# Kernel tuning notes

Hardware: AMD Instinct MI355X
Metric: run time of the kernel (lower is better)

## Reference

```python
import jax, jax.numpy as jnp
import numpy as np

B, T, UNITS, OUT = 64, 512, 512, 256
N_SPEED, N_HD = 20, 50
VMIN, VMAX = 0.0, 0.5


def setup_inputs() -> dict:
    key = jax.random.key(0)
    ks = jax.random.split(key, 9)
    # vel[..., 0] = speed in [0, 0.5], vel[..., 1] = head direction in [0, 2pi]
    u = jax.random.uniform(ks[0], (B, T, 2), dtype=jnp.float32)
    vel = u * jnp.array([VMAX, 2.0 * np.pi], dtype=jnp.float32)
    r = jax.random.normal(ks[1], (B, T, 2), dtype=jnp.float32)  # target positions
    start_state = 0.01 * jax.random.normal(ks[2], (1, UNITS), dtype=jnp.float32)
    # Dense kernels: RandomNormal(0, 0.001) for inputs, identity for recurrent
    W_speed = 0.001 * jax.random.normal(ks[3], (N_SPEED, UNITS), dtype=jnp.float32)
    W_hd = 0.001 * jax.random.normal(ks[4], (N_HD, UNITS), dtype=jnp.float32)
    W_rec = jnp.eye(UNITS, dtype=jnp.float32) + 0.001 * jax.random.normal(ks[5], (UNITS, UNITS), dtype=jnp.float32)
    b_rec = jnp.zeros((UNITS,), dtype=jnp.float32)
    W_out = (1.0 / np.sqrt(UNITS)) * jax.random.normal(ks[6], (UNITS, OUT), dtype=jnp.float32)
    b_out = jnp.zeros((OUT,), dtype=jnp.float32)
    return {"vel": vel, "r": r, "start_state": start_state, "W_speed": W_speed,
            "W_hd": W_hd, "W_rec": W_rec, "b_rec": b_rec, "W_out": W_out, "b_out": b_out}


def reference(vel, r, start_state, W_speed, W_hd, W_rec, b_rec, W_out, b_out):
    f32 = jnp.float32
    speed_centers = jnp.linspace(VMIN, VMAX, N_SPEED, dtype=f32)          # (20,)
    speed_sd = (VMAX - VMIN) / N_SPEED
    hd_centers = jnp.linspace(0.0, 2.0 * np.pi, N_HD, dtype=f32)          # (50,)
    kappa = f32(2.0 * np.pi)                                              # VonMises concentration

    # RBF features for all timesteps at once (the per-step fusable chain)
    speed_feat = jnp.exp((-0.5 / speed_sd ** 2) * (vel[..., 0, None] - speed_centers) ** 2)  # (B,T,20)
    # VonMises pdf: exp(k*cos(x-mu)) / (2*pi*I0(k)); use i0e for stability
    i0e_k = jax.scipy.special.i0e(kappa)
    hd_feat = jnp.exp(kappa * (jnp.cos(vel[..., 1, None] - hd_centers) - 1.0)) / (2.0 * np.pi * i0e_k)  # (B,T,50)

    # Input drive (speed_input + hd_input + recurrent bias), precomputed for all t
    drive = speed_feat @ W_speed + hd_feat @ W_hd + b_rec  # (B,T,U)

    h0 = jnp.broadcast_to(start_state, (vel.shape[0], start_state.shape[1]))  # start_state * ones((B,1))

    def step(h, d_t):
        h_new = jax.nn.relu(h @ W_rec + d_t)
        return h_new, h_new

    _, hs = jax.lax.scan(step, h0, jnp.swapaxes(drive, 0, 1))  # (T,B,U)
    rnn_states = jnp.swapaxes(hs, 0, 1)                         # (B,T,U)

    out = jax.nn.relu(rnn_states @ W_out + b_out)               # (B,T,N)
    ta = out / jnp.sum(out + 1e-10, axis=1, keepdims=True)      # normalize over time
    pa = out / jnp.sum(out + 1e-10, axis=2, keepdims=True)      # normalize over nodes

    expected_centers = jnp.einsum('btn,btd->bnd', ta, r)        # (B,N,2)
    expected_position = jnp.einsum('btn,bnd->btd', pa, expected_centers)  # (B,T,2)
    return expected_position
```

## Files before the change

### kernel.cpp

```cpp
#include <hip/hip_runtime.h>
#include <hip/hip_bf16.h>

#define BATCH 64
#define TT 512
#define UNITS 512
#define NOUT 256
#define NSPEED 20
#define NHD 50
#define NFEAT 70

#define SPEED_COEF (-800.0f)
#define SPEED_STEP (0.5f / 19.0f)
#define HD_STEP (6.28318530718f / 49.0f)
#define KAPPA 6.2831853f
#define C_HD 0.9783857f

#define GS 4
#define CPB 128

__global__ __launch_bounds__(256) void prep_w4s_kernel(
    const float* __restrict__ W, float4* __restrict__ wp,
    unsigned* __restrict__ cnt) {
  int idx = blockIdx.x * 256 + threadIdx.x;
  int s = idx >> 14, k4 = (idx >> 7) & 127, col = idx & 127;
  int gcol = s * CPB + col;
  const float* w0 = W + (size_t)(k4 * 4) * UNITS + gcol;
  wp[idx] = make_float4(w0[0], w0[UNITS], w0[2 * UNITS], w0[3 * UNITS]);
  if (idx < BATCH)
    __hip_atomic_store(&cnt[idx * 32], 0u, __ATOMIC_RELAXED,
                       __HIP_MEMORY_SCOPE_AGENT);
}

__global__ __launch_bounds__(256) void feat_drive_kernel(
    const float* __restrict__ vel, const float* __restrict__ W_speed,
    const float* __restrict__ W_hd, const float* __restrict__ b_rec,
    float* __restrict__ drive) {
  __shared__ float feats[64][NFEAT];
  const int row0 = blockIdx.x * 64;
  const int tid = threadIdx.x;

  for (int j = tid; j < 64 * NFEAT; j += 256) {
    int row = j / NFEAT, k = j % NFEAT;
    int grow = row0 + row;
    float f;
    if (k < NSPEED) {
      float s = vel[grow * 2 + 0];
      float d = s - (float)k * SPEED_STEP;
      f = __expf(SPEED_COEF * d * d);
    } else {
      float hd = vel[grow * 2 + 1];
      float c = (float)(k - NSPEED) * HD_STEP;
      f = C_HD * __expf(KAPPA * (__cosf(hd - c) - 1.0f));
    }
    feats[row][k] = f;
  }
  __syncthreads();

  const float2* Ws2 = (const float2*)W_speed;
  const float2* Wh2 = (const float2*)W_hd;
  float2 br = ((const float2*)b_rec)[tid];

  for (int rg = 0; rg < 8; ++rg) {
    float a0[8], a1[8];
#pragma unroll
    for (int j = 0; j < 8; ++j) {
      a0[j] = br.x;
      a1[j] = br.y;
    }
#pragma unroll 4
    for (int k = 0; k < NSPEED; ++k) {
      float2 w = Ws2[k * 256 + tid];
#pragma unroll
      for (int j = 0; j < 8; ++j) {
        float f = feats[rg * 8 + j][k];
        a0[j] = fmaf(f, w.x, a0[j]);
        a1[j] = fmaf(f, w.y, a1[j]);
      }
    }
#pragma unroll 5
    for (int k = 0; k < NHD; ++k) {
      float2 w = Wh2[k * 256 + tid];
#pragma unroll
      for (int j = 0; j < 8; ++j) {
        float f = feats[rg * 8 + j][NSPEED + k];
        a0[j] = fmaf(f, w.x, a0[j]);
        a1[j] = fmaf(f, w.y, a1[j]);
      }
    }
#pragma unroll
    for (int j = 0; j < 8; ++j)
      ((float2*)drive)[(size_t)(row0 + rg * 8 + j) * 256 + tid] =
          make_float2(a0[j], a1[j]);
  }
}

__global__ __launch_bounds__(1024) void rnn_scan6_kernel(
    const float4* __restrict__ wp, const float* __restrict__ drive,
    const float* __restrict__ start_state, float* __restrict__ hstates,
    unsigned* __restrict__ cnt) {
  __shared__ __align__(16) float hf[UNITS];
  __shared__ float pt[1024];
  const int bid = blockIdx.x;
  const int b = bid & 63, s = bid >> 6;
  const int tid = threadIdx.x;
  const int col = tid & (CPB - 1);
  const int kg = tid >> 7;
  const int scol = s * CPB + col;

  float4 w[16];
  {
    const float4* base = wp + (s << 14) + (kg << 11) + col;
#pragma unroll
    for (int i = 0; i < 16; ++i) w[i] = base[i << 7];
  }
  if (tid < 128) ((float4*)hf)[tid] = ((const float4*)start_state)[tid];
  __syncthreads();

  const float* D = drive + (size_t)b * TT * UNITS;
  float* H = hstates + (size_t)b * TT * UNITS;
  unsigned* c = cnt + (b << 5);

  for (int t = 0; t < TT; ++t) {
    const float4* hv = (const float4*)hf + (kg << 4);
    float a0 = 0.f, a1 = 0.f, a2 = 0.f, a3 = 0.f;
#pragma unroll
    for (int i = 0; i < 16; ++i) {
      float4 h4 = hv[i];
      a0 = fmaf(h4.x, w[i].x, a0);
      a1 = fmaf(h4.y, w[i].y, a1);
      a2 = fmaf(h4.z, w[i].z, a2);
      a3 = fmaf(h4.w, w[i].w, a3);
    }
    pt[tid] = (a0 + a1) + (a2 + a3);
    __syncthreads();
    if (tid < 128) {
      float sum = 0.f;
#pragma unroll
      for (int j = 0; j < 8; ++j) sum += pt[col + (j << 7)];
      float hn = fmaxf(sum + D[t * UNITS + scol], 0.0f);
      __hip_atomic_store(&H[t * UNITS + scol], hn, __ATOMIC_RELAXED,
                         __HIP_MEMORY_SCOPE_AGENT);
    }
    if (t == TT - 1) break;
    __syncthreads();
    if (tid == 0) {
      __hip_atomic_fetch_add(c, 1u, __ATOMIC_RELAXED,
                             __HIP_MEMORY_SCOPE_AGENT);
      unsigned tgt = (unsigned)(GS * (t + 1));
      while (__hip_atomic_load(c, __ATOMIC_RELAXED,
                               __HIP_MEMORY_SCOPE_AGENT) < tgt)
        __builtin_amdgcn_s_sleep(1);
    }
    __syncthreads();
    asm volatile("" ::: "memory");
    if (tid < 128) {
      unsigned long long p0 = __hip_atomic_load(
          (const unsigned long long*)&H[t * UNITS + tid * 4], __ATOMIC_RELAXED,
          __HIP_MEMORY_SCOPE_AGENT);
      unsigned long long p1 = __hip_atomic_load(
          (const unsigned long long*)&H[t * UNITS + tid * 4 + 2],
          __ATOMIC_RELAXED, __HIP_MEMORY_SCOPE_AGENT);
      float2 f0 = __builtin_bit_cast(float2, p0);
      float2 f1 = __builtin_bit_cast(float2, p1);
      ((float4*)hf)[tid] = make_float4(f0.x, f0.y, f1.x, f1.y);
    }
    __syncthreads();
  }
}

__global__ __launch_bounds__(256) void out_gemm_kernel(
    const float* __restrict__ A,
    const float* __restrict__ Bm,
    const float* __restrict__ b_out,
    float* __restrict__ C) {
  __shared__ float As[16][132];
  __shared__ float Bs[16][132];
  const int bm = blockIdx.x, bn = blockIdx.y;
  const int tid = threadIdx.x;
  const int tm = tid >> 4, tn = tid & 15;

  float acc[8][8] = {{0.f}};

  for (int k0 = 0; k0 < UNITS; k0 += 16) {
    {
      int ar = tid >> 2;
      int ak = (tid & 3) << 2;
      float4 v0 = *(const float4*)&A[(size_t)(bm * 128 + ar) * 512 + k0 + ak];
      float4 v1 =
          *(const float4*)&A[(size_t)(bm * 128 + ar + 64) * 512 + k0 + ak];
      As[ak + 0][ar] = v0.x;
      As[ak + 1][ar] = v0.y;
      As[ak + 2][ar] = v0.z;
      As[ak + 3][ar] = v0.w;
      As[ak + 0][ar + 64] = v1.x;
      As[ak + 1][ar + 64] = v1.y;
      As[ak + 2][ar + 64] = v1.z;
      As[ak + 3][ar + 64] = v1.w;
      int bk = tid >> 4;
      int bc = (tid & 15) << 3;
      float4 w0 = *(const float4*)&Bm[(size_t)(k0 + bk) * 256 + bn * 128 + bc];
      float4 w1 =
          *(const float4*)&Bm[(size_t)(k0 + bk) * 256 + bn * 128 + bc + 4];
      *(float4*)&Bs[bk][bc] = w0;
      *(float4*)&Bs[bk][bc + 4] = w1;
    }
    __syncthreads();
#pragma unroll
    for (int kk = 0; kk < 16; ++kk) {
      float4 a0 = *(const float4*)&As[kk][tm * 8];
      float4 a1 = *(const float4*)&As[kk][tm * 8 + 4];
      float4 b0 = *(const float4*)&Bs[kk][tn * 8];
      float4 b1 = *(const float4*)&Bs[kk][tn * 8 + 4];
      float av[8] = {a0.x, a0.y, a0.z, a0.w, a1.x, a1.y, a1.z, a1.w};
      float bv[8] = {b0.x, b0.y, b0.z, b0.w, b1.x, b1.y, b1.z, b1.w};
#pragma unroll
      for (int i = 0; i < 8; ++i)
#pragma unroll
        for (int j = 0; j < 8; ++j) acc[i][j] = fmaf(av[i], bv[j], acc[i][j]);
    }
    __syncthreads();
  }

  float4 bo0 = *(const float4*)&b_out[bn * 128 + tn * 8];
  float4 bo1 = *(const float4*)&b_out[bn * 128 + tn * 8 + 4];
  float bo[8] = {bo0.x, bo0.y, bo0.z, bo0.w, bo1.x, bo1.y, bo1.z, bo1.w};
#pragma unroll
  for (int i = 0; i < 8; ++i) {
    int row = bm * 128 + tm * 8 + i;
    float o[8];
#pragma unroll
    for (int j = 0; j < 8; ++j) o[j] = fmaxf(acc[i][j] + bo[j], 0.0f);
    float* cp = &C[(size_t)row * 256 + bn * 128 + tn * 8];
    *(float4*)cp = make_float4(o[0], o[1], o[2], o[3]);
    *(float4*)(cp + 4) = make_float4(o[4], o[5], o[6], o[7]);
  }
}

__global__ __launch_bounds__(256) void ec_kernel(
    const float* __restrict__ out, const float* __restrict__ r,
    float* __restrict__ EC) {
  const int b = blockIdx.x, n = threadIdx.x;
  const float* ob = out + (size_t)b * TT * NOUT;
  const float2* rb = (const float2*)r + (size_t)b * TT;
  float s = 0.0f, e0 = 0.0f, e1 = 0.0f;
  for (int t = 0; t < TT; ++t) {
    float o = ob[t * NOUT + n];
    float2 rv = rb[t];
    s += o;
    e0 = fmaf(o, rv.x, e0);
    e1 = fmaf(o, rv.y, e1);
  }
  float inv = 1.0f / (s + 5.12e-8f);
  ((float2*)EC)[b * NOUT + n] = make_float2(e0 * inv, e1 * inv);
}

__global__ __launch_bounds__(256) void ep_kernel(
    const float* __restrict__ out, const float* __restrict__ EC,
    float* __restrict__ EP) {
  const int b = blockIdx.x;
  const int tid = threadIdx.x;
  const int lane = tid & 63, wave = tid >> 6;
  __shared__ float ec0[NOUT], ec1[NOUT];

  float2 e = ((const float2*)EC)[b * NOUT + tid];
  ec0[tid] = e.x;
  ec1[tid] = e.y;
  __syncthreads();

  float4 c0 = *(const float4*)&ec0[lane * 4];
  float4 c1 = *(const float4*)&ec1[lane * 4];

  const float* ob = out + (size_t)b * TT * NOUT;
  float2* epb = (float2*)EP + (size_t)b * TT;

  for (int t = wave; t < TT; t += 4) {
    float4 o = *(const float4*)&ob[t * NOUT + lane * 4];
    float s = o.x + o.y + o.z + o.w;
    float a0 = o.x * c0.x + o.y * c0.y + o.z * c0.z + o.w * c0.w;
    float a1 = o.x * c1.x + o.y * c1.y + o.z * c1.z + o.w * c1.w;
#pragma unroll
    for (int off = 32; off > 0; off >>= 1) {
      s += __shfl_down(s, off);
      a0 += __shfl_down(a0, off);
      a1 += __shfl_down(a1, off);
    }
    if (lane == 0) {
      float inv = 1.0f / (s + 2.56e-8f);
      epb[t] = make_float2(a0 * inv, a1 * inv);
    }
  }
}

extern "C" void kernel_launch(void* const* d_in, const int* in_sizes, int n_in,
                              void* d_out, int out_size, void* d_ws,
                              size_t ws_size, hipStream_t stream) {
  const float* vel = (const float*)d_in[0];
  const float* r = (const float*)d_in[1];
  const float* start_state = (const float*)d_in[2];
  const float* W_speed = (const float*)d_in[3];
  const float* W_hd = (const float*)d_in[4];
  const float* W_rec = (const float*)d_in[5];
  const float* b_rec = (const float*)d_in[6];
  const float* W_out = (const float*)d_in[7];
  const float* b_out = (const float*)d_in[8];
  float* EP = (float*)d_out;

  char* ws = (char*)d_ws;
  float* drive = (float*)ws;
  float* hstates = (float*)(ws + (size_t)67108864);
  float* outbuf = (float*)ws;
  float4* wpack = (float4*)(ws + (size_t)134217728);
  unsigned* cnt = (unsigned*)(ws + (size_t)135266304);
  float* EC = (float*)(ws + (size_t)135274496);

  prep_w4s_kernel<<<256, 256, 0, stream>>>(W_rec, wpack, cnt);
  feat_drive_kernel<<<512, 256, 0, stream>>>(vel, W_speed, W_hd, b_rec, drive);
  rnn_scan6_kernel<<<256, 1024, 0, stream>>>(wpack, drive, start_state,
                                             hstates, cnt);
  out_gemm_kernel<<<dim3(256, 2), 256, 0, stream>>>(hstates, W_out, b_out,
                                                    outbuf);
  ec_kernel<<<64, 256, 0, stream>>>(outbuf, r, EC);
  ep_kernel<<<64, 256, 0, stream>>>(outbuf, EC, EP);
}
```

Measured before the change: 1.278 ms.

## Replace counter barrier in RNN scan with poison-flag dataflow sync on hidden states

Drops the per-batch atomic counter barrier, one of the two per-step __syncthreads, and the thread-0 spin loop. A new kernel first fills the hidden-state buffer with a poison bit pattern, and each block then polls directly for the three remote 128-column slices of h_t until they are no longer poison. Its own slice is written straight into shared memory. This cuts one round trip of inter-block signalling per timestep, at the cost of an extra 64MB fill pass and of depending on the assumption that no real value equals the poison pattern.

```diff
diff --git a/kernel.cpp b/kernel.cpp
--- a/kernel.cpp
+++ b/kernel.cpp
@@ -17,18 +17,24 @@
 
 #define GS 4
 #define CPB 128
+#define POISON 0xAAAAAAAAu
+
+__global__ __launch_bounds__(256) void clear_h_kernel(uint4* __restrict__ H) {
+  size_t i = (size_t)(blockIdx.x * 256 + threadIdx.x) * 4;
+  uint4 p = make_uint4(POISON, POISON, POISON, POISON);
+  H[i + 0] = p;
+  H[i + 1] = p;
+  H[i + 2] = p;
+  H[i + 3] = p;
+}
 
 __global__ __launch_bounds__(256) void prep_w4s_kernel(
-    const float* __restrict__ W, float4* __restrict__ wp,
-    unsigned* __restrict__ cnt) {
+    const float* __restrict__ W, float4* __restrict__ wp) {
   int idx = blockIdx.x * 256 + threadIdx.x;
   int s = idx >> 14, k4 = (idx >> 7) & 127, col = idx & 127;
   int gcol = s * CPB + col;
   const float* w0 = W + (size_t)(k4 * 4) * UNITS + gcol;
   wp[idx] = make_float4(w0[0], w0[UNITS], w0[2 * UNITS], w0[3 * UNITS]);
-  if (idx < BATCH)
-    __hip_atomic_store(&cnt[idx * 32], 0u, __ATOMIC_RELAXED,
-                       __HIP_MEMORY_SCOPE_AGENT);
 }
 
 __global__ __launch_bounds__(256) void feat_drive_kernel(
@@ -94,10 +100,9 @@
   }
 }
 
-__global__ __launch_bounds__(1024) void rnn_scan6_kernel(
+__global__ __launch_bounds__(1024) void rnn_scan8_kernel(
     const float4* __restrict__ wp, const float* __restrict__ drive,
-    const float* __restrict__ start_state, float* __restrict__ hstates,
-    unsigned* __restrict__ cnt) {
+    const float* __restrict__ start_state, float* __restrict__ hstates) {
   __shared__ __align__(16) float hf[UNITS];
   __shared__ float pt[1024];
   const int bid = blockIdx.x;
@@ -105,7 +110,7 @@
   const int tid = threadIdx.x;
   const int col = tid & (CPB - 1);
   const int kg = tid >> 7;
-  const int scol = s * CPB + col;
+  const int scol = (s << 7) + col;
 
   float4 w[16];
   {
@@ -118,7 +123,6 @@
 
   const float* D = drive + (size_t)b * TT * UNITS;
   float* H = hstates + (size_t)b * TT * UNITS;
-  unsigned* c = cnt + (b << 5);
 
   for (int t = 0; t < TT; ++t) {
     const float4* hv = (const float4*)hf + (kg << 4);
@@ -140,29 +144,25 @@
       float hn = fmaxf(sum + D[t * UNITS + scol], 0.0f);
       __hip_atomic_store(&H[t * UNITS + scol], hn, __ATOMIC_RELAXED,
                          __HIP_MEMORY_SCOPE_AGENT);
+      hf[scol] = hn;
     }
     if (t == TT - 1) break;
-    __syncthreads();
-    if (tid == 0) {
-      __hip_atomic_fetch_add(c, 1u, __ATOMIC_RELAXED,
-                             __HIP_MEMORY_SCOPE_AGENT);
-      unsigned tgt = (unsigned)(GS * (t + 1));
-      while (__hip_atomic_load(c, __ATOMIC_RELAXED,
-                               __HIP_MEMORY_SCOPE_AGENT) < tgt)
-        __builtin_amdgcn_s_sleep(1);
-    }
-    __syncthreads();
-    asm volatile("" ::: "memory");
-    if (tid < 128) {
-      unsigned long long p0 = __hip_atomic_load(
-          (const unsigned long long*)&H[t * UNITS + tid * 4], __ATOMIC_RELAXED,
-          __HIP_MEMORY_SCOPE_AGENT);
-      unsigned long long p1 = __hip_atomic_load(
-          (const unsigned long long*)&H[t * UNITS + tid * 4 + 2],
-          __ATOMIC_RELAXED, __HIP_MEMORY_SCOPE_AGENT);
-      float2 f0 = __builtin_bit_cast(float2, p0);
-      float2 f1 = __builtin_bit_cast(float2, p1);
-      ((float4*)hf)[tid] = make_float4(f0.x, f0.y, f1.x, f1.y);
+    if (tid < 96) {
+      int grp = tid < (s << 5) ? tid : tid + 32;
+      const unsigned long long* src =
+          (const unsigned long long*)&H[t * UNITS + (grp << 2)];
+      unsigned long long v0, v1;
+      do {
+        v0 = __hip_atomic_load(src, __ATOMIC_RELAXED,
+                               __HIP_MEMORY_SCOPE_AGENT);
+      } while ((unsigned)v0 == POISON || (unsigned)(v0 >> 32) == POISON);
+      do {
+        v1 = __hip_atomic_load(src + 1, __ATOMIC_RELAXED,
+                               __HIP_MEMORY_SCOPE_AGENT);
+      } while ((unsigned)v1 == POISON || (unsigned)(v1 >> 32) == POISON);
+      float2 f0 = __builtin_bit_cast(float2, v0);
+      float2 f1 = __builtin_bit_cast(float2, v1);
+      ((float4*)hf)[grp] = make_float4(f0.x, f0.y, f1.x, f1.y);
     }
     __syncthreads();
   }
@@ -310,13 +310,13 @@
   float* hstates = (float*)(ws + (size_t)67108864);
   float* outbuf = (float*)ws;
   float4* wpack = (float4*)(ws + (size_t)134217728);
-  unsigned* cnt = (unsigned*)(ws + (size_t)135266304);
   float* EC = (float*)(ws + (size_t)135274496);
 
-  prep_w4s_kernel<<<256, 256, 0, stream>>>(W_rec, wpack, cnt);
+  clear_h_kernel<<<4096, 256, 0, stream>>>((uint4*)hstates);
+  prep_w4s_kernel<<<256, 256, 0, stream>>>(W_rec, wpack);
   feat_drive_kernel<<<512, 256, 0, stream>>>(vel, W_speed, W_hd, b_rec, drive);
-  rnn_scan6_kernel<<<256, 1024, 0, stream>>>(wpack, drive, start_state,
-                                             hstates, cnt);
+  rnn_scan8_kernel<<<256, 1024, 0, stream>>>(wpack, drive, start_state,
+                                             hstates);
   out_gemm_kernel<<<dim3(256, 2), 256, 0, stream>>>(hstates, W_out, b_out,
                                                     outbuf);
   ec_kernel<<<64, 256, 0, stream>>>(outbuf, r, EC);
```

Result: faster. 1.253 ms (-2.0%).
